# Kernel tuning notes

Hardware: AMD Instinct MI355X
Metric: run time of the kernel (lower is better)

## Reference

```python
import jax, jax.numpy as jnp
import numpy as np

S = 64        # num_states
ODIM = 8      # padded neighbor-feature width
H = 256       # HIDDEN_DIM
A = 16        # num_actions
B = 16384     # batch (dtpt)
IDIM = S + ODIM
NEG_SLOPE = 0.01  # nn.LeakyReLU default
EPS = 1e-5        # nn.LayerNorm default


def setup_inputs() -> dict:
    key = jax.random.key(0)
    ks = jax.random.split(key, 8)
    x = jax.random.normal(ks[0], (B, S), jnp.float32)
    # per-state neighbor indices into x's feature dim, padded to ODIM with a mask
    o_idx = jax.random.randint(ks[1], (S, ODIM), 0, S)
    o_len = jax.random.randint(ks[2], (S,), 1, ODIM + 1)
    o_mask = jnp.arange(ODIM)[None, :] < o_len[:, None]  # [S, ODIM] bool

    def lin(k, fin, fout):
        bound = 1.0 / np.sqrt(fin)
        kw, kb = jax.random.split(k)
        W = jax.random.uniform(kw, (S, fin, fout), jnp.float32, -bound, bound)
        b = jax.random.uniform(kb, (S, fout), jnp.float32, -bound, bound)
        return W, b

    W1, b1 = lin(ks[3], IDIM, H)
    W2, b2 = lin(ks[4], H, H)
    Wp, bp = lin(ks[5], H, A)
    g1 = jnp.ones((S, H), jnp.float32); be1 = jnp.zeros((S, H), jnp.float32)
    g2 = jnp.ones((S, H), jnp.float32); be2 = jnp.zeros((S, H), jnp.float32)
    return dict(x=x, o_idx=o_idx, o_mask=o_mask, W1=W1, b1=b1, g1=g1, be1=be1,
                W2=W2, b2=b2, g2=g2, be2=be2, Wp=Wp, bp=bp)


def _layer_norm(h, g, b):
    # h: [B, S, H], per-state affine params g,b: [S, H]
    mu = jnp.mean(h, axis=-1, keepdims=True)
    var = jnp.mean((h - mu) ** 2, axis=-1, keepdims=True)
    return (h - mu) * jax.lax.rsqrt(var + EPS) * g[None] + b[None]


def reference(x, o_idx, o_mask, W1, b1, g1, be1, W2, b2, g2, be2, Wp, bp):
    # irregular gather: for each state s take x[:, o_nbr_index[s]], zero-pad to ODIM
    o = jnp.where(o_mask[None, :, :], x[:, o_idx], jnp.float32(0))  # [B, S, ODIM]
    one_hot = jnp.broadcast_to(jnp.eye(S, dtype=x.dtype)[None], (x.shape[0], S, S))
    inp = jnp.concatenate([one_hot, o], axis=-1)  # [B, S, IDIM]

    h = jnp.einsum('bsi,sih->bsh', inp, W1) + b1[None]
    h = _layer_norm(jax.nn.leaky_relu(h, NEG_SLOPE), g1, be1)
    h = jnp.einsum('bsh,shk->bsk', h, W2) + b2[None]
    h = _layer_norm(jax.nn.leaky_relu(h, NEG_SLOPE), g2, be2)
    pi_logit = jnp.einsum('bsh,sha->bsa', h, Wp) + bp[None]  # [B, S, A]
    lg_sm = jax.nn.log_softmax(pi_logit, axis=-1)
    return pi_logit, lg_sm
```

## Files before the change

### kernel.cpp

```cpp
#include <hip/hip_runtime.h>

#define LNEPS 1e-5f

typedef __attribute__((ext_vector_type(8)))  short          bf16x8;
typedef __attribute__((ext_vector_type(8)))  unsigned short u16x8;
typedef __attribute__((ext_vector_type(4)))  float          f32x4;
typedef __attribute__((ext_vector_type(16))) float          f32x16;
typedef __attribute__((ext_vector_type(4)))  unsigned int   u32x4;

#define MFMA32(a, b, c) __builtin_amdgcn_mfma_f32_32x32x16_bf16((a), (b), (c), 0, 0, 0)

#define WS_W2G  0
#define WS_A1   8388608
#define WS_WPG  8912896
#define WS_UC2  10027008
#define WS_MIDX 10092544

union U8 { bf16x8 v; unsigned u[4]; };

__device__ __forceinline__ unsigned short f2bf(float v) {
  union { float f; unsigned u; } a; a.f = v;
  unsigned r = a.u + 0x7fffu + ((a.u >> 16) & 1u);
  return (unsigned short)(r >> 16);
}
__device__ __forceinline__ unsigned cvtpk(float lo, float hi) {
  unsigned r;
  asm("v_cvt_pk_bf16_f32 %0, %1, %2" : "=v"(r) : "v"(lo), "v"(hi));
  return r;
}
__device__ __forceinline__ void swap2(unsigned& a, unsigned& b) {
  asm volatile("v_permlane32_swap_b32 %0, %1" : "+v"(a), "+v"(b));
}
__device__ __forceinline__ void plswap(unsigned w, unsigned& lo, unsigned& hi) {
  unsigned a = w, b = w;
  asm volatile("v_permlane32_swap_b32 %0, %1" : "+v"(a), "+v"(b));
  lo = a; hi = b;
}

__global__ void prep_midx_k(const int* __restrict__ oidx,
                            const unsigned* __restrict__ mask32,
                            int* __restrict__ midx) {
  __shared__ int fgt1, ffl;
  const int t = threadIdx.x;
  if (t == 0) { fgt1 = 0; ffl = 0; }
  __syncthreads();
  if (t < 128) {
    unsigned wv = mask32[t];
    if (wv == 0x3f800000u) atomicOr(&ffl, 1);
    else if (wv > 1u)      atomicOr(&fgt1, 1);
  }
  __syncthreads();
  const int mode = ffl ? 2 : (fgt1 ? 1 : 0);
  int mv;
  if (mode == 2)      mv = (((const float*)mask32)[t] != 0.0f) ? 1 : 0;
  else if (mode == 1) mv = (int)((const unsigned char*)mask32)[t];
  else                mv = ((const int*)mask32)[t];
  midx[t] = (mv != 0) ? oidx[t] : -1;
}

__global__ __launch_bounds__(256) void prep_w2g_k(
    const float* __restrict__ W2, const float* __restrict__ g1,
    unsigned short* __restrict__ w2g) {
  const int tid = blockIdx.x * 256 + threadIdx.x;
  const int l = tid & 63;
  const int t = (tid >> 6) & 15;
  const int i = (tid >> 10) & 7;
  const int s = tid >> 13;
  const int n = i * 32 + (l & 31);
  const int h = l >> 5;
  const float* w = W2 + (size_t)s * 65536;
  const float* g = g1 + s * 256;
  u16x8 v;
#pragma unroll
  for (int j = 0; j < 8; ++j) {
    const int k = t * 16 + h * 8 + j;
    v[j] = f2bf(w[k * 256 + n] * g[k]);
  }
  ((u16x8*)w2g)[tid] = v;
}

__global__ __launch_bounds__(256) void prep_uc2_k(
    const float* __restrict__ W2, const float* __restrict__ g1,
    const float* __restrict__ be1, const float* __restrict__ b2,
    unsigned* __restrict__ uc2) {
  const int tid = blockIdx.x * 256 + threadIdx.x;
  const int s = tid >> 8, n = tid & 255;
  const float* w = W2 + (size_t)s * 65536 + n;
  const float* g = g1 + s * 256;
  const float* be = be1 + s * 256;
  float u = 0.f, c = 0.f;
#pragma unroll 8
  for (int k = 0; k < 256; ++k) {
    const float wk = w[k * 256];
    u = fmaf(wk, g[k], u);
    c = fmaf(wk, be[k], c);
  }
  c += b2[tid];
  uc2[tid] = (unsigned)f2bf(u) | ((unsigned)f2bf(c) << 16);
}

__global__ __launch_bounds__(256) void prep_a1_k(
    const float* __restrict__ W1, const float* __restrict__ b1,
    unsigned short* __restrict__ a1b) {
  const int tid = blockIdx.x * 256 + threadIdx.x;
  const int l = tid & 63;
  const int i = (tid >> 6) & 7;
  const int s = tid >> 9;
  const int n = i * 32 + (l & 31);
  const float* w = W1 + (size_t)s * 72 * 256;
  u16x8 v;
#pragma unroll
  for (int j = 0; j < 8; ++j) v[j] = 0;
  if (l < 32) {
#pragma unroll
    for (int j = 0; j < 8; ++j) v[j] = f2bf(w[(64 + j) * 256 + n]);
  } else {
    v[0] = f2bf(w[s * 256 + n] + b1[s * 256 + n]);
  }
  ((u16x8*)a1b)[tid] = v;
}

__global__ __launch_bounds__(256) void prep_wpg_k(
    const float* __restrict__ Wp, const float* __restrict__ g2,
    const float* __restrict__ be2, const float* __restrict__ bp,
    unsigned short* __restrict__ wpg) {
  const int tid = blockIdx.x * 256 + threadIdx.x;
  const int l = tid & 63;
  const int r = tid >> 6;
  const int t = r % 17;
  const int s = r / 17;
  const int a = l & 31;
  const int h = l >> 5;
  u16x8 v;
#pragma unroll
  for (int j = 0; j < 8; ++j) v[j] = 0;
  if (t < 16) {
    if (a < 16) {
      const float* w = Wp + (size_t)s * 4096;
      const float* g = g2 + s * 256;
#pragma unroll
      for (int j = 0; j < 8; ++j) {
        const int k = t * 16 + h * 8 + j;
        v[j] = f2bf(w[k * 16 + a] * g[k]);
      }
    }
  } else if (h == 0 && a < 16) {
    const float* w = Wp + (size_t)s * 4096;
    float up = 0.f, cp = 0.f;
#pragma unroll 8
    for (int k = 0; k < 256; ++k) {
      const float wk = w[k * 16 + a];
      up = fmaf(wk, g2[s * 256 + k], up);
      cp = fmaf(wk, be2[s * 256 + k], cp);
    }
    cp += bp[s * 16 + a];
    v[0] = f2bf(up); v[1] = f2bf(cp);
  }
  ((u16x8*)wpg)[tid] = v;
}

__device__ __forceinline__ void pack_tile(const f32x16& a,
                                          unsigned* f0, unsigned* f1) {
  unsigned w0 = cvtpk(a[0], a[1]),   w1 = cvtpk(a[2], a[3]);
  unsigned w2 = cvtpk(a[4], a[5]),   w3 = cvtpk(a[6], a[7]);
  unsigned w4 = cvtpk(a[8], a[9]),   w5 = cvtpk(a[10], a[11]);
  unsigned w6 = cvtpk(a[12], a[13]), w7 = cvtpk(a[14], a[15]);
  swap2(w0, w2); swap2(w1, w3); swap2(w4, w6); swap2(w5, w7);
  f0[0] = w0; f0[1] = w1; f0[2] = w2; f0[3] = w3;
  f1[0] = w4; f1[1] = w5; f1[2] = w6; f1[3] = w7;
}

__global__ __launch_bounds__(512, 2) void actor_main(
    const float* __restrict__ x, const int* __restrict__ midx,
    const unsigned short* __restrict__ w2g, const unsigned* __restrict__ uc2,
    const unsigned short* __restrict__ a1b, const unsigned short* __restrict__ wpg,
    float* __restrict__ out) {
  extern __shared__ char lds[];
  const int tid = threadIdx.x;
  const int wv = tid >> 6;
  const int l = tid & 63;
  const int bl = l & 31;
  const int h = l >> 5;
  const int s = blockIdx.x >> 2;
  const int rowstart = (blockIdx.x & 3) << 12;

  {
    const u32x4* src = (const u32x4*)(w2g + (size_t)s * 65536);
    u32x4* dst = (u32x4*)lds;
#pragma unroll
    for (int i = 0; i < 16; ++i) dst[i * 512 + tid] = src[i * 512 + tid];
  }

  unsigned aext[8];
#pragma unroll
  for (int i = 0; i < 8; ++i) {
    const unsigned t = uc2[(s * 8 + i) * 32 + bl];
    aext[i] = h ? 0u : t;
  }
  const int4 mi4 = ((const int4*)(midx + s * 8))[h];
  const bf16x8* A1 = ((const bf16x8*)a1b) + (size_t)(s * 8) * 64 + l;
  const bf16x8* A3 = ((const bf16x8*)wpg) + (size_t)(s * 17) * 64 + l;
  const char* ldsl = lds + (l << 4);

  const float* xbase = x + (size_t)(rowstart + wv * 32 + bl) * 64;

  float ga = mi4.x < 0 ? 0.f : xbase[mi4.x];
  float gb = mi4.y < 0 ? 0.f : xbase[mi4.y];
  float gc = mi4.z < 0 ? 0.f : xbase[mi4.z];
  float gd = mi4.w < 0 ? 0.f : xbase[mi4.w];

  __syncthreads();

  for (int it = 0; it < 16; ++it) {
    const int row = rowstart + it * 256 + wv * 32 + bl;

    unsigned oa0, ob0, oa1, ob1;
    plswap(cvtpk(ga, gb), oa0, ob0);
    plswap(cvtpk(gc, gd), oa1, ob1);
    U8 B1;
    B1.u[0] = h ? 0x00003F80u : oa0;
    B1.u[1] = h ? 0u : oa1;
    B1.u[2] = h ? 0u : ob0;
    B1.u[3] = h ? 0u : ob1;

    {
      const float* xn = xbase + (size_t)(((it + 1) & 15) * 256) * 64;
      ga = mi4.x < 0 ? 0.f : xn[mi4.x];
      gb = mi4.y < 0 ? 0.f : xn[mi4.y];
      gc = mi4.z < 0 ? 0.f : xn[mi4.z];
      gd = mi4.w < 0 ? 0.f : xn[mi4.w];
    }

    float s0 = 0.f, s1 = 0.f, q0 = 0.f, q1 = 0.f;
    f32x16 acc2[8];
    bf16x8 a1n = A1[0];
    bf16x8 Afc[8];
#pragma unroll
    for (int j = 0; j < 8; ++j)
      Afc[j] = *(const bf16x8*)(ldsl + ((j * 16 + 0) << 10));

#pragma unroll
    for (int i = 0; i < 8; ++i) {
      f32x16 z = {};
      const f32x16 accP = MFMA32(a1n, B1.v, z);
      if (i < 7) a1n = A1[(i + 1) * 64];

      f32x16 yv;
#pragma unroll
      for (int r = 0; r < 16; ++r) {
        float v = accP[r];
        v = fmaxf(v, 0.01f * v);
        yv[r] = v;
        if (r & 1) { s1 += v; q1 = fmaf(v, v, q1); }
        else       { s0 += v; q0 = fmaf(v, v, q0); }
      }
      U8 Bf0, Bf1;
      pack_tile(yv, Bf0.u, Bf1.u);

#pragma unroll
      for (int j = 0; j < 8; ++j) {
        if (i == 0) { f32x16 zz = {}; acc2[j] = MFMA32(Afc[j], Bf0.v, zz); }
        else        { acc2[j] = MFMA32(Afc[j], Bf0.v, acc2[j]); }
      }
      bf16x8 Afn[8];
#pragma unroll
      for (int j = 0; j < 8; ++j)
        Afn[j] = *(const bf16x8*)(ldsl + ((j * 16 + 2 * i + 1) << 10));
#pragma unroll
      for (int j = 0; j < 8; ++j) acc2[j] = MFMA32(Afn[j], Bf1.v, acc2[j]);
      if (i < 7) {
#pragma unroll
        for (int j = 0; j < 8; ++j)
          Afc[j] = *(const bf16x8*)(ldsl + ((j * 16 + 2 * i + 2) << 10));
      }
    }

    float sum = s0 + s1, ssq = q0 + q1;
    sum += __shfl_xor(sum, 32, 64);
    ssq += __shfl_xor(ssq, 32, 64);
    const float m1 = sum * 0.00390625f;
    const float var1 = fmaf(ssq, 0.00390625f, -m1 * m1) + LNEPS;
    const float rho1 = rsqrtf(var1);
    const float std1 = var1 * rho1;
    const unsigned be2w = cvtpk(-m1, std1);
    bf16x8 p0 = A3[0], p1 = A3[64];
    {
      U8 Bx; Bx.u[0] = h ? 0u : be2w; Bx.u[1] = 0; Bx.u[2] = 0; Bx.u[3] = 0;
#pragma unroll
      for (int i = 0; i < 8; ++i) {
        U8 Ax; Ax.u[0] = aext[i]; Ax.u[1] = 0; Ax.u[2] = 0; Ax.u[3] = 0;
        acc2[i] = MFMA32(Ax.v, Bx.v, acc2[i]);
      }
    }

    f32x16 a3a = {}, a3b = {};
    s0 = s1 = q0 = q1 = 0.f;
#pragma unroll
    for (int i = 0; i < 8; ++i) {
      bf16x8 n0, n1;
      if (i < 7) { n0 = A3[(2 * i + 2) * 64]; n1 = A3[(2 * i + 3) * 64]; }
      else       { n0 = A3[16 * 64]; n1 = p1; }
      f32x16 yv;
#pragma unroll
      for (int r = 0; r < 16; ++r) {
        float v = acc2[i][r];
        v = fmaxf(v, 0.01f * v);
        yv[r] = v;
        if (r & 1) { s1 += v; q1 = fmaf(v, v, q1); }
        else       { s0 += v; q0 = fmaf(v, v, q0); }
      }
      U8 Bf0, Bf1;
      pack_tile(yv, Bf0.u, Bf1.u);
      a3a = MFMA32(p0, Bf0.v, a3a);
      a3b = MFMA32(p1, Bf1.v, a3b);
      p0 = n0; p1 = n1;
    }
    float sum2 = s0 + s1, ssq2 = q0 + q1;
    sum2 += __shfl_xor(sum2, 32, 64);
    ssq2 += __shfl_xor(ssq2, 32, 64);
    const float mp = sum2 * 0.00390625f;
    const float qp = ssq2 * 0.00390625f;
    const float var2 = rho1 * rho1 * fmaf(-mp, mp, qp) + LNEPS;
    const float rho2 = rsqrtf(var2);
    const float sigma = rho1 * rho2;
    const float inv = var2 * rho2 * std1;
    const unsigned be3w = cvtpk(-mp, inv);
    {
      U8 Bx; Bx.u[0] = h ? 0u : be3w; Bx.u[1] = 0; Bx.u[2] = 0; Bx.u[3] = 0;
      a3a = MFMA32(p0, Bx.v, a3a);
    }

    float lg[8];
#pragma unroll
    for (int r = 0; r < 8; ++r) lg[r] = sigma * (a3a[r] + a3b[r]);
    float mx = fmaxf(fmaxf(fmaxf(lg[0], lg[1]), fmaxf(lg[2], lg[3])),
                     fmaxf(fmaxf(lg[4], lg[5]), fmaxf(lg[6], lg[7])));
    mx = fmaxf(mx, __shfl_xor(mx, 32, 64));
    float es = 0.f;
#pragma unroll
    for (int r = 0; r < 8; ++r) es += __expf(lg[r] - mx);
    es += __shfl_xor(es, 32, 64);
    const float lse = mx + __logf(es);

    const size_t ob = (((size_t)row << 6) + s) * 16 + (h << 2);
    f32x4 v0 = {lg[0], lg[1], lg[2], lg[3]};
    f32x4 v1 = {lg[4], lg[5], lg[6], lg[7]};
    *(f32x4*)(out + ob) = v0;
    *(f32x4*)(out + ob + 8) = v1;
    f32x4 w0 = {lg[0] - lse, lg[1] - lse, lg[2] - lse, lg[3] - lse};
    f32x4 w1 = {lg[4] - lse, lg[5] - lse, lg[6] - lse, lg[7] - lse};
    *(f32x4*)(out + 16777216 + ob) = w0;
    *(f32x4*)(out + 16777216 + ob + 8) = w1;
  }
}

extern "C" void kernel_launch(void* const* d_in, const int* in_sizes, int n_in,
                              void* d_out, int out_size, void* d_ws, size_t ws_size,
                              hipStream_t stream) {
  const float* x    = (const float*)d_in[0];
  const int*   oidx = (const int*)d_in[1];
  const unsigned* omask = (const unsigned*)d_in[2];
  const float* W1 = (const float*)d_in[3];
  const float* b1 = (const float*)d_in[4];
  const float* g1 = (const float*)d_in[5];
  const float* be1 = (const float*)d_in[6];
  const float* W2 = (const float*)d_in[7];
  const float* b2 = (const float*)d_in[8];
  const float* g2 = (const float*)d_in[9];
  const float* be2 = (const float*)d_in[10];
  const float* Wp = (const float*)d_in[11];
  const float* bp = (const float*)d_in[12];
  float* out = (float*)d_out;

  char* ws = (char*)d_ws;
  unsigned short* wsW2G = (unsigned short*)(ws + WS_W2G);
  unsigned short* wsA1  = (unsigned short*)(ws + WS_A1);
  unsigned short* wsWPG = (unsigned short*)(ws + WS_WPG);
  unsigned*       wsUC2 = (unsigned*)(ws + WS_UC2);
  int*            wsMIDX = (int*)(ws + WS_MIDX);

  prep_midx_k<<<1, 512, 0, stream>>>(oidx, omask, wsMIDX);
  prep_w2g_k<<<2048, 256, 0, stream>>>(W2, g1, wsW2G);
  prep_uc2_k<<<64, 256, 0, stream>>>(W2, g1, be1, b2, wsUC2);
  prep_a1_k<<<128, 256, 0, stream>>>(W1, b1, wsA1);
  prep_wpg_k<<<272, 256, 0, stream>>>(Wp, g2, be2, bp, wsWPG);

  hipFuncSetAttribute((const void*)actor_main,
                      hipFuncAttributeMaxDynamicSharedMemorySize, 131072);
  actor_main<<<256, 512, 131072, stream>>>(
      x, wsMIDX, wsW2G, wsUC2, wsA1, wsWPG, out);
}
```

Baseline: 272.3 us.

## Pre-gather neighbor features into packed bf16 buffer and software-pipeline layer-1 MFMA

Adds a prep kernel that gathers the masked neighbor features for every state and row into a contiguous packed-bf16 workspace buffer (64x16384 x 16 bytes). The main kernel then issues one coalesced 16-byte load per row instead of four scattered fp32 gathers plus conversion and permlane swaps. It also issues the layer-1 MFMA for the next tile one step ahead so its latency overlaps the activation and packing work. In exchange it adds an extra kernel launch and about 16 MB of workspace write and read traffic.

Result: slower. 288.9 us (+6.1%).

```diff
diff --git a/kernel.cpp b/kernel.cpp
--- a/kernel.cpp
+++ b/kernel.cpp
@@ -15,6 +15,7 @@
 #define WS_WPG  8912896
 #define WS_UC2  10027008
 #define WS_MIDX 10092544
+#define WS_XG   10094592
 
 union U8 { bf16x8 v; unsigned u[4]; };
 
@@ -30,11 +31,6 @@
 }
 __device__ __forceinline__ void swap2(unsigned& a, unsigned& b) {
   asm volatile("v_permlane32_swap_b32 %0, %1" : "+v"(a), "+v"(b));
-}
-__device__ __forceinline__ void plswap(unsigned w, unsigned& lo, unsigned& hi) {
-  unsigned a = w, b = w;
-  asm volatile("v_permlane32_swap_b32 %0, %1" : "+v"(a), "+v"(b));
-  lo = a; hi = b;
 }
 
 __global__ void prep_midx_k(const int* __restrict__ oidx,
@@ -56,6 +52,24 @@
   else if (mode == 1) mv = (int)((const unsigned char*)mask32)[t];
   else                mv = ((const int*)mask32)[t];
   midx[t] = (mv != 0) ? oidx[t] : -1;
+}
+
+__global__ __launch_bounds__(256) void prep_xg_k(
+    const float* __restrict__ x, const int* __restrict__ midx,
+    u32x4* __restrict__ xg) {
+  const int g = blockIdx.x * 256 + threadIdx.x;
+  const int s = g >> 14, row = g & 16383;
+  const float* xr = x + (size_t)row * 64;
+  const int* mi = midx + s * 8;
+  u32x4 w;
+#pragma unroll
+  for (int p = 0; p < 4; ++p) {
+    const int m0 = mi[2 * p], m1 = mi[2 * p + 1];
+    const float a = m0 < 0 ? 0.f : xr[m0];
+    const float b = m1 < 0 ? 0.f : xr[m1];
+    w[p] = (unsigned)f2bf(a) | ((unsigned)f2bf(b) << 16);
+  }
+  xg[g] = w;
 }
 
 __global__ __launch_bounds__(256) void prep_w2g_k(
@@ -171,7 +185,7 @@
 }
 
 __global__ __launch_bounds__(512, 2) void actor_main(
-    const float* __restrict__ x, const int* __restrict__ midx,
+    const u32x4* __restrict__ xg,
     const unsigned short* __restrict__ w2g, const unsigned* __restrict__ uc2,
     const unsigned short* __restrict__ a1b, const unsigned short* __restrict__ wpg,
     float* __restrict__ out) {
@@ -197,54 +211,41 @@
     const unsigned t = uc2[(s * 8 + i) * 32 + bl];
     aext[i] = h ? 0u : t;
   }
-  const int4 mi4 = ((const int4*)(midx + s * 8))[h];
   const bf16x8* A1 = ((const bf16x8*)a1b) + (size_t)(s * 8) * 64 + l;
   const bf16x8* A3 = ((const bf16x8*)wpg) + (size_t)(s * 17) * 64 + l;
   const char* ldsl = lds + (l << 4);
-
-  const float* xbase = x + (size_t)(rowstart + wv * 32 + bl) * 64;
-
-  float ga = mi4.x < 0 ? 0.f : xbase[mi4.x];
-  float gb = mi4.y < 0 ? 0.f : xbase[mi4.y];
-  float gc = mi4.z < 0 ? 0.f : xbase[mi4.z];
-  float gd = mi4.w < 0 ? 0.f : xbase[mi4.w];
+  const u32x4* XG = xg + ((size_t)s << 14);
+
+  const int rbase = rowstart + wv * 32 + bl;
+
+  u32x4 gcur = XG[rbase];
 
   __syncthreads();
 
   for (int it = 0; it < 16; ++it) {
-    const int row = rowstart + it * 256 + wv * 32 + bl;
-
-    unsigned oa0, ob0, oa1, ob1;
-    plswap(cvtpk(ga, gb), oa0, ob0);
-    plswap(cvtpk(gc, gd), oa1, ob1);
+    const int row = rbase + it * 256;
+
     U8 B1;
-    B1.u[0] = h ? 0x00003F80u : oa0;
-    B1.u[1] = h ? 0u : oa1;
-    B1.u[2] = h ? 0u : ob0;
-    B1.u[3] = h ? 0u : ob1;
-
-    {
-      const float* xn = xbase + (size_t)(((it + 1) & 15) * 256) * 64;
-      ga = mi4.x < 0 ? 0.f : xn[mi4.x];
-      gb = mi4.y < 0 ? 0.f : xn[mi4.y];
-      gc = mi4.z < 0 ? 0.f : xn[mi4.z];
-      gd = mi4.w < 0 ? 0.f : xn[mi4.w];
-    }
+    B1.u[0] = h ? 0x00003F80u : gcur[0];
+    B1.u[1] = h ? 0u : gcur[1];
+    B1.u[2] = h ? 0u : gcur[2];
+    B1.u[3] = h ? 0u : gcur[3];
+
+    gcur = XG[rbase + ((it + 1) & 15) * 256];
 
     float s0 = 0.f, s1 = 0.f, q0 = 0.f, q1 = 0.f;
     f32x16 acc2[8];
-    bf16x8 a1n = A1[0];
+    bf16x8 a1n = A1[64];
     bf16x8 Afc[8];
 #pragma unroll
     for (int j = 0; j < 8; ++j)
       Afc[j] = *(const bf16x8*)(ldsl + ((j * 16 + 0) << 10));
 
+    f32x16 accP;
+    { f32x16 z = {}; accP = MFMA32(A1[0], B1.v, z); }
+
 #pragma unroll
     for (int i = 0; i < 8; ++i) {
-      f32x16 z = {};
-      const f32x16 accP = MFMA32(a1n, B1.v, z);
-      if (i < 7) a1n = A1[(i + 1) * 64];
-
       f32x16 yv;
 #pragma unroll
       for (int r = 0; r < 16; ++r) {
@@ -256,6 +257,12 @@
       }
       U8 Bf0, Bf1;
       pack_tile(yv, Bf0.u, Bf1.u);
+
+      if (i < 7) {
+        f32x16 z = {};
+        accP = MFMA32(a1n, B1.v, z);
+        if (i < 6) a1n = A1[(i + 2) * 64];
+      }
 
 #pragma unroll
       for (int j = 0; j < 8; ++j) {
@@ -378,8 +385,10 @@
   unsigned short* wsWPG = (unsigned short*)(ws + WS_WPG);
   unsigned*       wsUC2 = (unsigned*)(ws + WS_UC2);
   int*            wsMIDX = (int*)(ws + WS_MIDX);
+  u32x4*          wsXG   = (u32x4*)(ws + WS_XG);
 
   prep_midx_k<<<1, 512, 0, stream>>>(oidx, omask, wsMIDX);
+  prep_xg_k<<<4096, 256, 0, stream>>>(x, wsMIDX, wsXG);
   prep_w2g_k<<<2048, 256, 0, stream>>>(W2, g1, wsW2G);
   prep_uc2_k<<<64, 256, 0, stream>>>(W2, g1, be1, b2, wsUC2);
   prep_a1_k<<<128, 256, 0, stream>>>(W1, b1, wsA1);
@@ -388,5 +397,5 @@
   hipFuncSetAttribute((const void*)actor_main,
                       hipFuncAttributeMaxDynamicSharedMemorySize, 131072);
   actor_main<<<256, 512, 131072, stream>>>(
-      x, wsMIDX, wsW2G, wsUC2, wsA1, wsWPG, out);
-}
+      wsXG, wsW2G, wsUC2, wsA1, wsWPG, out);
+}
```
